# Kernel tuning notes

Hardware: AMD Instinct MI355X
Metric: run time of the kernel (lower is better)

Reference implementation:

```python
import jax, jax.numpy as jnp
import numpy as np

B, N, IN_DIM, HID, OUT, E = 2, 50000, 64, 256, 128, 500000

def setup_inputs() -> dict:
    key = jax.random.key(0)
    ks = jax.random.split(key, 8)
    s = lambda fan_in: 1.0 / np.sqrt(fan_in)
    x = jax.random.normal(ks[0], (B, N, IN_DIM), dtype=jnp.float32)
    edges = jax.random.randint(ks[1], (E, 2), 0, N, dtype=jnp.int64)
    return {
        "x": x,
        "edges": edges,
        "ew1": jax.random.normal(ks[2], (2 * IN_DIM, HID), dtype=jnp.float32) * s(2 * IN_DIM),
        "eb1": jnp.zeros((HID,), jnp.float32),
        "ew2": jax.random.normal(ks[3], (HID, OUT), dtype=jnp.float32) * s(HID),
        "eb2": jnp.zeros((OUT,), jnp.float32),
        "nw1": jax.random.normal(ks[4], (IN_DIM, HID), dtype=jnp.float32) * s(IN_DIM),
        "nb1": jnp.zeros((HID,), jnp.float32),
        "nw2": jax.random.normal(ks[5], (HID, OUT), dtype=jnp.float32) * s(HID),
        "nb2": jnp.zeros((OUT,), jnp.float32),
        "dw": jax.random.normal(ks[6], (OUT, IN_DIM), dtype=jnp.float32) * s(OUT),
        "db": jnp.zeros((IN_DIM,), jnp.float32),
    }

def _mlp(z, w1, b1, w2, b2):
    return jax.nn.relu(z @ w1 + b1) @ w2 + b2

def reference(x, edges, ew1, eb1, ew2, eb2, nw1, nb1, nw2, nb2, dw, db):
    u, v = edges[:, 0], edges[:, 1]
    # node embedding: [B, N, OUT]
    h = _mlp(x, nw1, nb1, nw2, nb2)
    # per-edge MLP on concatenated endpoint features: [B, E, OUT]
    edge_input = jnp.concatenate([x[:, u], x[:, v]], axis=-1)  # [B, E, 2*IN]
    edge_emb = _mlp(edge_input, ew1, eb1, ew2, eb2)
    # scatter-add edge message to both endpoints
    messages = jnp.zeros_like(h).at[:, u].add(edge_emb).at[:, v].add(edge_emb)
    h = h + messages
    recon = h @ dw + db  # [B, N, IN]
    return recon
```

## Files before the change

kernel.cpp:

```cpp
#include <hip/hip_runtime.h>
#include <hip/hip_bf16.h>

#define BB   2
#define NN   50000
#define BN   100000
#define NE   500000
#define NSB  196

#define EPITCH 136
#define XPITCH 72
#define HPITCH 264

using u16 = unsigned short;
using u32 = unsigned int;
typedef __attribute__((ext_vector_type(8))) short short8;
typedef __attribute__((ext_vector_type(4))) short short4v;
typedef __attribute__((ext_vector_type(4))) float f32x4;

__device__ __forceinline__ u16 f2bf(float f) {
    union { float f; u32 u; } w; w.f = f;
    return (u16)((w.u + 0x7fffu + ((w.u >> 16) & 1u)) >> 16);
}

__global__ __launch_bounds__(256) void csr_zero(int* __restrict__ cursor) {
    int i = blockIdx.x * 256 + threadIdx.x;
    if (i < NN) cursor[i] = 0;
}

__global__ __launch_bounds__(256) void csr_hist(const int* __restrict__ edges,
                                                int* __restrict__ cursor) {
    int e = blockIdx.x * 256 + threadIdx.x;
    if (e < NE) {
        atomicAdd(&cursor[edges[2*e]], 1);
        atomicAdd(&cursor[edges[2*e+1]], 1);
    }
}

__global__ __launch_bounds__(256) void scan_pass1(const int* __restrict__ cursor,
                                                  int* __restrict__ bsum) {
    __shared__ int s[256];
    const int t = threadIdx.x;
    int i = blockIdx.x * 256 + t;
    s[t] = (i < NN) ? cursor[i] : 0;
    __syncthreads();
    for (int d = 128; d > 0; d >>= 1) {
        if (t < d) s[t] += s[t + d];
        __syncthreads();
    }
    if (t == 0) bsum[blockIdx.x] = s[0];
}

__global__ __launch_bounds__(256) void scan_pass2(const int* __restrict__ bsum,
                                                  int* __restrict__ boff) {
    __shared__ int s[256];
    const int t = threadIdx.x;
    s[t] = (t < NSB) ? bsum[t] : 0;
    __syncthreads();
    for (int d = 1; d < 256; d <<= 1) {
        int v = (t >= d) ? s[t - d] : 0;
        __syncthreads();
        s[t] += v;
        __syncthreads();
    }
    if (t <= NSB) boff[t] = (t == 0) ? 0 : s[t - 1];
}

__global__ __launch_bounds__(256) void scan_pass3(int* __restrict__ cursor,
                                                  const int* __restrict__ boff,
                                                  int* __restrict__ off) {
    __shared__ int s[256];
    const int t = threadIdx.x;
    int i = blockIdx.x * 256 + t;
    int v = (i < NN) ? cursor[i] : 0;
    s[t] = v;
    __syncthreads();
    for (int d = 1; d < 256; d <<= 1) {
        int p = (t >= d) ? s[t - d] : 0;
        __syncthreads();
        s[t] += p;
        __syncthreads();
    }
    int excl = boff[blockIdx.x] + s[t] - v;
    if (i < NN) { off[i] = excl; cursor[i] = excl; }
    if (i == NN - 1) off[NN] = excl + v;
}

__global__ __launch_bounds__(256) void csr_fill(const int* __restrict__ edges,
                                                int* __restrict__ cursor,
                                                int* __restrict__ inc) {
    int e = blockIdx.x * 256 + threadIdx.x;
    if (e < NE) {
        int pu = atomicAdd(&cursor[edges[2*e]], 1);   inc[pu] = e;
        int pv = atomicAdd(&cursor[edges[2*e+1]], 1); inc[pv] = e;
    }
}

__global__ __launch_bounds__(256) void swizzle_w1(
    const float* __restrict__ ew1, const float* __restrict__ nw1,
    u16* __restrict__ frag)
{
    int idx = blockIdx.x * 256 + threadIdx.x;
    if (idx >= 49152) return;
    const float* src; int KB, local;
    if (idx < 32768) { local = idx;         src = ew1; KB = 4; }
    else             { local = idx - 32768; src = nw1; KB = 2; }
    int j = local & 7, l = (local >> 3) & 63, rest = local >> 9;
    int kblk = rest % KB, ntile = rest / KB;
    int n = ntile * 16 + (l & 15);
    int k = kblk * 32 + ((l >> 4) << 3) + j;
    frag[idx] = f2bf(src[k * 256 + n]);
}

__global__ __launch_bounds__(256) void fuse_w2(
    const float* __restrict__ ew2, const float* __restrict__ nw2,
    const float* __restrict__ dw, u16* __restrict__ frag)
{
    int idx = blockIdx.x * 256 + threadIdx.x;
    if (idx >= 32768) return;
    const float* src = (idx < 16384) ? ew2 : nw2;
    int local = idx & 16383;
    int j = local & 7, l = (local >> 3) & 63, rest = local >> 9;
    int kblk = rest & 7, ntile = rest >> 3;
    int n = ntile * 16 + (l & 15);
    int k = kblk * 32 + ((l >> 4) << 3) + j;
    float s = 0.f;
    for (int jj = 0; jj < 128; ++jj) s = fmaf(src[k * 128 + jj], dw[jj * 64 + n], s);
    frag[49152 + idx] = f2bf(s);
}

__global__ __launch_bounds__(64) void fuse_bias(
    const float* __restrict__ eb2, const float* __restrict__ nb2,
    const float* __restrict__ dw, const float* __restrict__ db,
    float* __restrict__ bias2)
{
    int d = threadIdx.x;
    float se = 0.f, sn = 0.f;
    for (int j = 0; j < 128; ++j) {
        float w = dw[j * 64 + d];
        se = fmaf(eb2[j], w, se);
        sn = fmaf(nb2[j], w, sn);
    }
    bias2[d] = se;
    bias2[64 + d] = sn + db[d];
}

__global__ __launch_bounds__(256) void x_to_bf16(const float* __restrict__ x,
                                                 u16* __restrict__ xbf)
{
    int i = blockIdx.x * 256 + threadIdx.x;
    if (i >= BN * 16) return;
    float4 g = ((const float4*)x)[i];
    short4v s;
    s.x = (short)f2bf(g.x); s.y = (short)f2bf(g.y);
    s.z = (short)f2bf(g.z); s.w = (short)f2bf(g.w);
    *(short4v*)(xbf + (size_t)i * 4) = s;
}

__global__ __launch_bounds__(256) void node_mlp_kernel(
    const u16* __restrict__ xbf, const float* __restrict__ nb1,
    const float* __restrict__ bias2, const u16* __restrict__ frag,
    float* __restrict__ out)
{
    __shared__ u16 xs[64 * XPITCH];
    __shared__ u16 hid[64 * HPITCH];
    const int t = threadIdx.x;
    const int wave = t >> 6, l = t & 63, lane15 = l & 15, quad = l >> 4;
    const int r0 = blockIdx.x * 64;
    const int valid = min(64, BN - r0);

    #pragma unroll
    for (int it = 0; it < 2; ++it) {
        int i = t + it * 256;
        int m = i >> 3, c8 = i & 7;
        int row = min(r0 + m, BN - 1);
        uint4 q = ((const uint4*)xbf)[(size_t)row * 8 + c8];
        *(uint4*)(xs + m * XPITCH + c8 * 8) = q;
    }
    __syncthreads();

    {
        f32x4 acc[4][4];
        #pragma unroll
        for (int i = 0; i < 4; ++i)
            #pragma unroll
            for (int mt = 0; mt < 4; ++mt) acc[i][mt] = f32x4{0.f,0.f,0.f,0.f};
        const u16* w1 = frag + 32768;
        #pragma unroll
        for (int kblk = 0; kblk < 2; ++kblk) {
            short8 bf[4], af[4];
            #pragma unroll
            for (int mt = 0; mt < 4; ++mt)
                bf[mt] = *(const short8*)(xs + (mt*16 + lane15) * XPITCH + kblk*32 + quad*8);
            #pragma unroll
            for (int i = 0; i < 4; ++i)
                af[i] = *(const short8*)(w1 + (((wave*4 + i)*2 + kblk)*64 + l) * 8);
            #pragma unroll
            for (int i = 0; i < 4; ++i)
                #pragma unroll
                for (int mt = 0; mt < 4; ++mt)
                    acc[i][mt] = __builtin_amdgcn_mfma_f32_16x16x32_bf16(af[i], bf[mt], acc[i][mt], 0, 0, 0);
        }
        #pragma unroll
        for (int i = 0; i < 4; ++i) {
            int n0 = (wave*4 + i)*16 + quad*4;
            float4 bv = *(const float4*)(nb1 + n0);
            #pragma unroll
            for (int mt = 0; mt < 4; ++mt) {
                int m = mt*16 + lane15;
                short4v s;
                s.x = (short)f2bf(fmaxf(acc[i][mt][0] + bv.x, 0.f));
                s.y = (short)f2bf(fmaxf(acc[i][mt][1] + bv.y, 0.f));
                s.z = (short)f2bf(fmaxf(acc[i][mt][2] + bv.z, 0.f));
                s.w = (short)f2bf(fmaxf(acc[i][mt][3] + bv.w, 0.f));
                *(short4v*)(hid + m * HPITCH + n0) = s;
            }
        }
    }
    __syncthreads();

    {
        f32x4 acc[4];
        #pragma unroll
        for (int mt = 0; mt < 4; ++mt) acc[mt] = f32x4{0.f,0.f,0.f,0.f};
        const u16* w2 = frag + 65536;
        #pragma unroll
        for (int kblk = 0; kblk < 8; ++kblk) {
            short8 bf[4], af;
            #pragma unroll
            for (int mt = 0; mt < 4; ++mt)
                bf[mt] = *(const short8*)(hid + (mt*16 + lane15) * HPITCH + kblk*32 + quad*8);
            af = *(const short8*)(w2 + ((wave*8 + kblk)*64 + l) * 8);
            #pragma unroll
            for (int mt = 0; mt < 4; ++mt)
                acc[mt] = __builtin_amdgcn_mfma_f32_16x16x32_bf16(af, bf[mt], acc[mt], 0, 0, 0);
        }
        int n0 = wave*16 + quad*4;
        float4 bv = *(const float4*)(bias2 + 64 + n0);
        #pragma unroll
        for (int mt = 0; mt < 4; ++mt) {
            int m = mt*16 + lane15;
            if (m < valid) {
                float4 o;
                o.x = acc[mt][0] + bv.x; o.y = acc[mt][1] + bv.y;
                o.z = acc[mt][2] + bv.z; o.w = acc[mt][3] + bv.w;
                *(float4*)(out + (size_t)(r0 + m) * 64 + n0) = o;
            }
        }
    }
}

__global__ __launch_bounds__(256) void edge_emb_kernel(
    const u16* __restrict__ xbf, const int* __restrict__ edges,
    const float* __restrict__ eb1, const float* __restrict__ bias2,
    const u16* __restrict__ frag, u16* __restrict__ edec)
{
    __shared__ u16 ein[64 * EPITCH];
    __shared__ u16 hid[64 * HPITCH];
    __shared__ int us[64], vs[64];
    const int t = threadIdx.x;
    const int wave = t >> 6, l = t & 63, lane15 = l & 15, quad = l >> 4;
    const int b = blockIdx.y;
    const int e0 = blockIdx.x * 64;
    const int valid = min(64, NE - e0);

    if (t < 64) {
        int e = min(e0 + t, NE - 1);
        us[t] = edges[2 * e];
        vs[t] = edges[2 * e + 1];
    }
    __syncthreads();

    #pragma unroll
    for (int it = 0; it < 4; ++it) {
        int i = t + it * 256;
        int m = i >> 4, c = i & 15;
        int half = c >> 3, c8 = c & 7;
        int node = half ? vs[m] : us[m];
        uint4 q = ((const uint4*)xbf)[(size_t)(b * NN + node) * 8 + c8];
        *(uint4*)(ein + m * EPITCH + half * 64 + c8 * 8) = q;
    }
    __syncthreads();

    {
        f32x4 acc[4][4];
        #pragma unroll
        for (int i = 0; i < 4; ++i)
            #pragma unroll
            for (int mt = 0; mt < 4; ++mt) acc[i][mt] = f32x4{0.f,0.f,0.f,0.f};
        const u16* w1 = frag;
        #pragma unroll
        for (int kblk = 0; kblk < 4; ++kblk) {
            short8 bf[4], af[4];
            #pragma unroll
            for (int mt = 0; mt < 4; ++mt)
                bf[mt] = *(const short8*)(ein + (mt*16 + lane15) * EPITCH + kblk*32 + quad*8);
            #pragma unroll
            for (int i = 0; i < 4; ++i)
                af[i] = *(const short8*)(w1 + (((wave*4 + i)*4 + kblk)*64 + l) * 8);
            #pragma unroll
            for (int i = 0; i < 4; ++i)
                #pragma unroll
                for (int mt = 0; mt < 4; ++mt)
                    acc[i][mt] = __builtin_amdgcn_mfma_f32_16x16x32_bf16(af[i], bf[mt], acc[i][mt], 0, 0, 0);
        }
        #pragma unroll
        for (int i = 0; i < 4; ++i) {
            int n0 = (wave*4 + i)*16 + quad*4;
            float4 bv = *(const float4*)(eb1 + n0);
            #pragma unroll
            for (int mt = 0; mt < 4; ++mt) {
                int m = mt*16 + lane15;
                short4v s;
                s.x = (short)f2bf(fmaxf(acc[i][mt][0] + bv.x, 0.f));
                s.y = (short)f2bf(fmaxf(acc[i][mt][1] + bv.y, 0.f));
                s.z = (short)f2bf(fmaxf(acc[i][mt][2] + bv.z, 0.f));
                s.w = (short)f2bf(fmaxf(acc[i][mt][3] + bv.w, 0.f));
                *(short4v*)(hid + m * HPITCH + n0) = s;
            }
        }
    }
    __syncthreads();

    {
        f32x4 acc[4];
        #pragma unroll
        for (int mt = 0; mt < 4; ++mt) acc[mt] = f32x4{0.f,0.f,0.f,0.f};
        const u16* w2 = frag + 49152;
        #pragma unroll
        for (int kblk = 0; kblk < 8; ++kblk) {
            short8 bf[4], af;
            #pragma unroll
            for (int mt = 0; mt < 4; ++mt)
                bf[mt] = *(const short8*)(hid + (mt*16 + lane15) * HPITCH + kblk*32 + quad*8);
            af = *(const short8*)(w2 + ((wave*8 + kblk)*64 + l) * 8);
            #pragma unroll
            for (int mt = 0; mt < 4; ++mt)
                acc[mt] = __builtin_amdgcn_mfma_f32_16x16x32_bf16(af, bf[mt], acc[mt], 0, 0, 0);
        }
        int n0 = wave*16 + quad*4;
        float4 bv = *(const float4*)(bias2 + n0);
        #pragma unroll
        for (int mt = 0; mt < 4; ++mt) {
            int m = mt*16 + lane15;
            if (m < valid) {
                short4v s;
                s.x = (short)f2bf(acc[mt][0] + bv.x);
                s.y = (short)f2bf(acc[mt][1] + bv.y);
                s.z = (short)f2bf(acc[mt][2] + bv.z);
                s.w = (short)f2bf(acc[mt][3] + bv.w);
                *(short4v*)(edec + ((size_t)b * NE + e0 + m) * 64 + n0) = s;
            }
        }
    }
}

__global__ __launch_bounds__(256) void gather_kernel(
    const u32* __restrict__ edec32, const int* __restrict__ off,
    const int* __restrict__ inc, float* __restrict__ out)
{
    const int t = threadIdx.x, wave = t >> 6, l = t & 63;
    const int b = blockIdx.y;
    const int n = blockIdx.x * 4 + wave;
    const int base = off[n], cnt = off[n + 1] - base;
    if (cnt == 0) return;
    const int half = l >> 5, c = l & 31;
    const u32* eb = edec32 + (size_t)b * NE * 32;
    float a0 = 0.f, a1 = 0.f;
    for (int j0 = 0; j0 < cnt; j0 += 64) {
        int ev = inc[min(base + j0 + l, 2 * NE - 1)];
        int lim = min(64, cnt - j0);
        for (int i = 0; i < lim; i += 2) {
            int sel = i + half;
            int e = __shfl(ev, sel);
            u32 w = eb[(size_t)e * 32 + c];
            union { u32 u; float f; } lo, hi;
            lo.u = w << 16; hi.u = w & 0xffff0000u;
            if (sel < lim) { a0 += lo.f; a1 += hi.f; }
        }
    }
    a0 += __shfl_xor(a0, 32);
    a1 += __shfl_xor(a1, 32);
    if (l < 32) {
        float2* p = (float2*)(out + (size_t)(b * NN + n) * 64 + 2 * c);
        float2 h = *p; h.x += a0; h.y += a1; *p = h;
    }
}

extern "C" void kernel_launch(void* const* d_in, const int* in_sizes, int n_in,
                              void* d_out, int out_size, void* d_ws, size_t ws_size,
                              hipStream_t stream) {
    const float* x     = (const float*)d_in[0];
    const int*   edges = (const int*)d_in[1];
    const float* ew1   = (const float*)d_in[2];
    const float* eb1   = (const float*)d_in[3];
    const float* ew2   = (const float*)d_in[4];
    const float* eb2   = (const float*)d_in[5];
    const float* nw1   = (const float*)d_in[6];
    const float* nb1   = (const float*)d_in[7];
    const float* nw2   = (const float*)d_in[8];
    const float* nb2   = (const float*)d_in[9];
    const float* dw    = (const float*)d_in[10];
    const float* db    = (const float*)d_in[11];
    float* out = (float*)d_out;

    char* w = (char*)d_ws;
    size_t o = 0;
    auto take = [&](size_t bytes) { char* p = w + o; o = (o + bytes + 511) & ~(size_t)511; return p; };
    u16*   frag   = (u16*)  take(81920 * 2);
    float* bias2  = (float*)take(128 * 4);
    int*   cursor = (int*)  take((size_t)NN * 4);
    int*   off    = (int*)  take((size_t)(NN + 1) * 4);
    int*   bsum   = (int*)  take((size_t)(NSB + 1) * 4);
    int*   boff   = (int*)  take((size_t)(NSB + 1) * 4);
    int*   inc    = (int*)  take((size_t)2 * NE * 4);
    u16*   xbf    = (u16*)  take((size_t)BN * 64 * 2);
    u16*   edec   = (u16*)  take((size_t)BB * NE * 64 * 2);

    csr_zero<<<NSB, 256, 0, stream>>>(cursor);
    csr_hist<<<(NE + 255) / 256, 256, 0, stream>>>(edges, cursor);
    scan_pass1<<<NSB, 256, 0, stream>>>(cursor, bsum);
    scan_pass2<<<1, 256, 0, stream>>>(bsum, boff);
    scan_pass3<<<NSB, 256, 0, stream>>>(cursor, boff, off);
    csr_fill<<<(NE + 255) / 256, 256, 0, stream>>>(edges, cursor, inc);

    swizzle_w1<<<192, 256, 0, stream>>>(ew1, nw1, frag);
    fuse_w2<<<128, 256, 0, stream>>>(ew2, nw2, dw, frag);
    fuse_bias<<<1, 64, 0, stream>>>(eb2, nb2, dw, db, bias2);
    x_to_bf16<<<(BN * 16 + 255) / 256, 256, 0, stream>>>(x, xbf);

    node_mlp_kernel<<<(BN + 63) / 64, 256, 0, stream>>>(xbf, nb1, bias2, frag, out);

    edge_emb_kernel<<<dim3((NE + 63) / 64, BB), 256, 0, stream>>>(xbf, edges, eb1, bias2, frag, edec);
    gather_kernel<<<dim3(NN / 4, BB), 256, 0, stream>>>((const u32*)edec, off, inc, out);
}
```

Baseline: 491.5 us.

## Scatter edge embeddings into CSR order so gather reads contiguous rows

The CSR fill now records each edge endpoint's slot position instead of an incidence list. The edge kernel stages its bf16 results in shared memory, then writes each edge row twice, once to each endpoint's CSR slot. The gather kernel then streams contiguous rows per node with no indirection. Batches are processed one at a time to reuse a single permuted buffer. This doubles edge-output writes (scattered 128B rows) and adds launches, in exchange for removing random reads in the gather.

Result: faster. 465.4 us (-5.3%).

```diff
diff --git a/kernel.cpp b/kernel.cpp
--- a/kernel.cpp
+++ b/kernel.cpp
@@ -10,6 +10,7 @@
 #define EPITCH 136
 #define XPITCH 72
 #define HPITCH 264
+#define RPITCH 72
 
 using u16 = unsigned short;
 using u32 = unsigned int;
@@ -87,11 +88,11 @@
 
 __global__ __launch_bounds__(256) void csr_fill(const int* __restrict__ edges,
                                                 int* __restrict__ cursor,
-                                                int* __restrict__ inc) {
+                                                int* __restrict__ pos) {
     int e = blockIdx.x * 256 + threadIdx.x;
     if (e < NE) {
-        int pu = atomicAdd(&cursor[edges[2*e]], 1);   inc[pu] = e;
-        int pv = atomicAdd(&cursor[edges[2*e+1]], 1); inc[pv] = e;
+        pos[2*e]     = atomicAdd(&cursor[edges[2*e]], 1);
+        pos[2*e + 1] = atomicAdd(&cursor[edges[2*e+1]], 1);
     }
 }
 
@@ -252,14 +253,14 @@
 __global__ __launch_bounds__(256) void edge_emb_kernel(
     const u16* __restrict__ xbf, const int* __restrict__ edges,
     const float* __restrict__ eb1, const float* __restrict__ bias2,
-    const u16* __restrict__ frag, u16* __restrict__ edec)
+    const u16* __restrict__ frag, const int* __restrict__ pos,
+    u16* __restrict__ perm, int b)
 {
     __shared__ u16 ein[64 * EPITCH];
     __shared__ u16 hid[64 * HPITCH];
-    __shared__ int us[64], vs[64];
+    __shared__ int us[64], vs[64], ps[64], qs[64];
     const int t = threadIdx.x;
     const int wave = t >> 6, l = t & 63, lane15 = l & 15, quad = l >> 4;
-    const int b = blockIdx.y;
     const int e0 = blockIdx.x * 64;
     const int valid = min(64, NE - e0);
 
@@ -267,6 +268,8 @@
         int e = min(e0 + t, NE - 1);
         us[t] = edges[2 * e];
         vs[t] = edges[2 * e + 1];
+        ps[t] = pos[2 * e];
+        qs[t] = pos[2 * e + 1];
     }
     __syncthreads();
 
@@ -342,47 +345,59 @@
         #pragma unroll
         for (int mt = 0; mt < 4; ++mt) {
             int m = mt*16 + lane15;
-            if (m < valid) {
-                short4v s;
-                s.x = (short)f2bf(acc[mt][0] + bv.x);
-                s.y = (short)f2bf(acc[mt][1] + bv.y);
-                s.z = (short)f2bf(acc[mt][2] + bv.z);
-                s.w = (short)f2bf(acc[mt][3] + bv.w);
-                *(short4v*)(edec + ((size_t)b * NE + e0 + m) * 64 + n0) = s;
-            }
+            short4v s;
+            s.x = (short)f2bf(acc[mt][0] + bv.x);
+            s.y = (short)f2bf(acc[mt][1] + bv.y);
+            s.z = (short)f2bf(acc[mt][2] + bv.z);
+            s.w = (short)f2bf(acc[mt][3] + bv.w);
+            *(short4v*)(ein + m * RPITCH + n0) = s;
+        }
+    }
+    __syncthreads();
+
+    #pragma unroll
+    for (int it = 0; it < 4; ++it) {
+        int i = t + it * 256;
+        int dest = i >> 3, c8 = i & 7;
+        int m = dest >> 1;
+        if (m < valid) {
+            int p = (dest & 1) ? qs[m] : ps[m];
+            ((uint4*)(perm + (size_t)p * 64))[c8] = *(const uint4*)(ein + m * RPITCH + c8 * 8);
         }
     }
 }
 
 __global__ __launch_bounds__(256) void gather_kernel(
-    const u32* __restrict__ edec32, const int* __restrict__ off,
-    const int* __restrict__ inc, float* __restrict__ out)
+    const u32* __restrict__ perm32, const int* __restrict__ off,
+    float* __restrict__ out, int b)
 {
     const int t = threadIdx.x, wave = t >> 6, l = t & 63;
-    const int b = blockIdx.y;
     const int n = blockIdx.x * 4 + wave;
     const int base = off[n], cnt = off[n + 1] - base;
     if (cnt == 0) return;
-    const int half = l >> 5, c = l & 31;
-    const u32* eb = edec32 + (size_t)b * NE * 32;
-    float a0 = 0.f, a1 = 0.f;
-    for (int j0 = 0; j0 < cnt; j0 += 64) {
-        int ev = inc[min(base + j0 + l, 2 * NE - 1)];
-        int lim = min(64, cnt - j0);
-        for (int i = 0; i < lim; i += 2) {
-            int sel = i + half;
-            int e = __shfl(ev, sel);
-            u32 w = eb[(size_t)e * 32 + c];
-            union { u32 u; float f; } lo, hi;
-            lo.u = w << 16; hi.u = w & 0xffff0000u;
-            if (sel < lim) { a0 += lo.f; a1 += hi.f; }
-        }
-    }
-    a0 += __shfl_xor(a0, 32);
-    a1 += __shfl_xor(a1, 32);
-    if (l < 32) {
-        float2* p = (float2*)(out + (size_t)(b * NN + n) * 64 + 2 * c);
-        float2 h = *p; h.x += a0; h.y += a1; *p = h;
+    const int slot = l >> 4, c8h = l & 15;
+    float a0 = 0.f, a1 = 0.f, a2 = 0.f, a3 = 0.f;
+    for (int j0 = 0; j0 < cnt; j0 += 4) {
+        int j = j0 + slot;
+        size_t r = (size_t)(base + min(j, cnt - 1));
+        const u32* rp = perm32 + r * 32 + 2 * c8h;
+        u32 w0 = rp[0], w1 = rp[1];
+        if (j < cnt) {
+            union { u32 u; float f; } x0, x1, x2, x3;
+            x0.u = w0 << 16; x1.u = w0 & 0xffff0000u;
+            x2.u = w1 << 16; x3.u = w1 & 0xffff0000u;
+            a0 += x0.f; a1 += x1.f; a2 += x2.f; a3 += x3.f;
+        }
+    }
+    a0 += __shfl_xor(a0, 16); a1 += __shfl_xor(a1, 16);
+    a2 += __shfl_xor(a2, 16); a3 += __shfl_xor(a3, 16);
+    a0 += __shfl_xor(a0, 32); a1 += __shfl_xor(a1, 32);
+    a2 += __shfl_xor(a2, 32); a3 += __shfl_xor(a3, 32);
+    if (l < 16) {
+        float4* p = (float4*)(out + (size_t)(b * NN + n) * 64 + 4 * l);
+        float4 h = *p;
+        h.x += a0; h.y += a1; h.z += a2; h.w += a3;
+        *p = h;
     }
 }
 
@@ -412,16 +427,16 @@
     int*   off    = (int*)  take((size_t)(NN + 1) * 4);
     int*   bsum   = (int*)  take((size_t)(NSB + 1) * 4);
     int*   boff   = (int*)  take((size_t)(NSB + 1) * 4);
-    int*   inc    = (int*)  take((size_t)2 * NE * 4);
+    int*   pos    = (int*)  take((size_t)2 * NE * 4);
     u16*   xbf    = (u16*)  take((size_t)BN * 64 * 2);
-    u16*   edec   = (u16*)  take((size_t)BB * NE * 64 * 2);
+    u16*   perm   = (u16*)  take((size_t)2 * NE * 64 * 2);
 
     csr_zero<<<NSB, 256, 0, stream>>>(cursor);
     csr_hist<<<(NE + 255) / 256, 256, 0, stream>>>(edges, cursor);
     scan_pass1<<<NSB, 256, 0, stream>>>(cursor, bsum);
     scan_pass2<<<1, 256, 0, stream>>>(bsum, boff);
     scan_pass3<<<NSB, 256, 0, stream>>>(cursor, boff, off);
-    csr_fill<<<(NE + 255) / 256, 256, 0, stream>>>(edges, cursor, inc);
+    csr_fill<<<(NE + 255) / 256, 256, 0, stream>>>(edges, cursor, pos);
 
     swizzle_w1<<<192, 256, 0, stream>>>(ew1, nw1, frag);
     fuse_w2<<<128, 256, 0, stream>>>(ew2, nw2, dw, frag);
@@ -430,6 +445,8 @@
 
     node_mlp_kernel<<<(BN + 63) / 64, 256, 0, stream>>>(xbf, nb1, bias2, frag, out);
 
-    edge_emb_kernel<<<dim3((NE + 63) / 64, BB), 256, 0, stream>>>(xbf, edges, eb1, bias2, frag, edec);
-    gather_kernel<<<dim3(NN / 4, BB), 256, 0, stream>>>((const u32*)edec, off, inc, out);
-}
+    for (int b = 0; b < BB; ++b) {
+        edge_emb_kernel<<<(NE + 63) / 64, 256, 0, stream>>>(xbf, edges, eb1, bias2, frag, pos, perm, b);
+        gather_kernel<<<NN / 4, 256, 0, stream>>>((const u32*)perm, off, out, b);
+    }
+}
```
